# Performance work log

Measured on AMD Instinct MI355X. Metric: run time of the kernel, lower is better.

The kernel has to match this reference:

```python
import jax, jax.numpy as jnp
import numpy as np

# Static sizes (match input_specs / init_kwargs)
N = 10000       # nodes
E = 160000      # edges
L = 2           # num_layers
S = 256         # scalar_dim (hidden_dim)
V = 32          # vec_dim (1o and 1e channel count)
L2 = 16         # 2e channel count
NRBF = 16
TDIM = 128
ESD = NRBF + 16 + 20 + 8 + S + S + TDIM   # 700 edge-scalar dim
WOUT = S + 4 * V + L2                     # 400 per-edge TP path weights
ADA = 2 * S + 2 * V + L2                  # 592 AdaLN modulation dim
FEAT = S + 3 * V + 3 * V + 5 * L2         # 528 flattened irreps width
DEG_INV = 1.0 / np.sqrt(E / N)            # 1/sqrt(avg degree) message normalizer


def setup_inputs() -> dict:
    key = jax.random.key(0)
    ks = jax.random.split(key, 30)
    f32 = jnp.float32

    def nrm(k, shape, scale=1.0):
        return jax.random.normal(k, shape, dtype=f32) * scale

    inp = {
        "h": nrm(ks[0], (N, FEAT)),
        "coords": nrm(ks[1], (N, 3), 3.0),
        "edge_ref_dist": jax.random.uniform(ks[2], (E,), dtype=f32) * 4.0,
        "t_emb": nrm(ks[3], (N, TDIM)),
        # per-layer learned params, stacked on leading L axis
        "etype_emb": nrm(ks[4], (L, 9, 16), 0.5),
        "btype_emb": nrm(ks[5], (L, 6, 8), 0.5),
        "bconj_emb": nrm(ks[6], (L, 3, 4), 0.5),
        "bring_emb": nrm(ks[7], (L, 3, 4), 0.5),
        "bstereo_emb": nrm(ks[8], (L, 5, 4), 0.5),
        "ref_W": nrm(ks[9], (L, 3, 8), 1.0 / np.sqrt(3)),
        "ref_b": jnp.zeros((L, 8), f32),
        "edge_W": nrm(ks[10], (L, ESD, WOUT), 1.0 / np.sqrt(ESD)),
        "edge_b": jnp.zeros((L, WOUT), f32),
        "sv_W": nrm(ks[11], (L, S, V), 1.0 / np.sqrt(S)),
        "proj_s": nrm(ks[12], (L, S, S), 1.0 / np.sqrt(S)),
        "proj_v1": nrm(ks[13], (L, V, V), 1.0 / np.sqrt(V)),
        "proj_v2": nrm(ks[14], (L, V, V), 1.0 / np.sqrt(V)),
        "proj_l2": nrm(ks[15], (L, L2, L2), 1.0 / np.sqrt(L2)),
        "ada_W": nrm(ks[16], (L, TDIM, ADA), 1.0 / np.sqrt(TDIM)),
        "ada_b": jnp.zeros((L, ADA), f32),
        # int graph structure
        "edge_index": jax.random.randint(ks[17], (2, E), 0, N),
        "edge_type": jax.random.randint(ks[18], (E,), 0, 9),
        "edge_bond_type": jax.random.randint(ks[19], (E,), 0, 6),
        "edge_bond_conjugated": jax.random.randint(ks[20], (E,), 0, 3),
        "edge_bond_in_ring": jax.random.randint(ks[21], (E,), 0, 3),
        "edge_bond_stereo": jax.random.randint(ks[22], (E,), 0, 5),
    }
    return inp


def _forward(h, coords, edge_ref_dist, t_emb,
             etype_emb, btype_emb, bconj_emb, bring_emb, bstereo_emb,
             ref_W, ref_b, edge_W, edge_b, sv_W,
             proj_s, proj_v1, proj_v2, proj_l2, ada_W, ada_b,
             edge_index, edge_type, edge_bond_type,
             edge_bond_conjugated, edge_bond_in_ring, edge_bond_stereo):
    src, dst = edge_index[0], edge_index[1]
    # geometry (shared across layers)
    diff = coords[dst] - coords[src]                    # [E,3]
    dist = jnp.linalg.norm(diff, axis=-1)               # [E]
    centers = jnp.linspace(0.0, 10.0, NRBF)
    width = 10.0 / NRBF
    rbf = jnp.exp(-(((dist[:, None] - centers) / width) ** 2))   # [E,NRBF]
    Y1 = diff / (dist[:, None] + 1e-8)                  # unit direction, l=1 SH
    has_ref = (edge_ref_dist > 0).astype(jnp.float32)
    delta = dist - edge_ref_dist
    ref_feat = jnp.stack([jnp.abs(delta), delta, has_ref], axis=-1)  # [E,3]

    for l in range(L):
        # split irreps blocks
        s = h[:, :S]
        v1o = h[:, S:S + 3 * V].reshape(N, V, 3)
        v1e = h[:, S + 3 * V:S + 6 * V].reshape(N, V, 3)
        q2e = h[:, S + 6 * V:].reshape(N, L2, 5)

        # edge scalar features (embeddings + RBF + node scalars + time)
        e_type = etype_emb[l][edge_type]
        e_bond = jnp.concatenate([
            btype_emb[l][edge_bond_type], bconj_emb[l][edge_bond_conjugated],
            bring_emb[l][edge_bond_in_ring], bstereo_emb[l][edge_bond_stereo]], axis=-1)
        e_ref = ref_feat @ ref_W[l] + ref_b[l]
        edge_scalars = jnp.concatenate(
            [rbf, e_type, e_bond, e_ref, s[src], s[dst], t_emb[dst]], axis=-1)  # [E,700]

        # per-edge tensor-product path weights
        w = edge_scalars @ edge_W[l] + edge_b[l]          # [E,400]
        w_s, w_v1, w_sv, w_v2, w_cx, w_l2 = jnp.split(
            w, [S, S + V, S + 2 * V, S + 3 * V, S + 4 * V], axis=-1)

        sv = s @ sv_W[l]                                  # [N,V] scalar->vec gate channels
        # equivariant messages
        m_s = w_s * s[src]                                                   # 0e x 0e -> 0e
        m_v1o = w_v1[:, :, None] * v1o[src] \
              + (w_sv * sv[src])[:, :, None] * Y1[:, None, :]                # 0e x 1o -> 1o
        m_v1e = w_v2[:, :, None] * v1e[src] \
              + w_cx[:, :, None] * jnp.cross(v1o[src], Y1[:, None, :])       # 1o x 1o -> 1e
        m_l2 = w_l2[:, :, None] * q2e[src]                                   # 0e x 2e -> 2e

        # scatter-sum to destination nodes
        agg_s = jax.ops.segment_sum(m_s, dst, num_segments=N) * DEG_INV
        agg_v1o = jax.ops.segment_sum(m_v1o, dst, num_segments=N) * DEG_INV
        agg_v1e = jax.ops.segment_sum(m_v1e, dst, num_segments=N) * DEG_INV
        agg_l2 = jax.ops.segment_sum(m_l2, dst, num_segments=N) * DEG_INV

        # per-irrep channel-mixing projection, scalar activation
        u_s = jax.nn.silu(agg_s @ proj_s[l])
        u_v1o = jnp.einsum('nci,cd->ndi', agg_v1o, proj_v1[l])
        u_v1e = jnp.einsum('nci,cd->ndi', agg_v1e, proj_v2[l])
        u_l2 = jnp.einsum('nci,cd->ndi', agg_l2, proj_l2[l])

        # residual
        s = s + u_s
        v1o = v1o + u_v1o
        v1e = v1e + u_v1e
        q2e = q2e + u_l2

        # equivariant AdaLN conditioned on t_emb
        ada = t_emb @ ada_W[l] + ada_b[l]
        sc, sh_, g1, g2, gl = jnp.split(ada, [S, 2 * S, 2 * S + V, 2 * S + 2 * V], axis=-1)
        mu = s.mean(axis=-1, keepdims=True)
        var = s.var(axis=-1, keepdims=True)
        s = (s - mu) / jnp.sqrt(var + 1e-5) * (1.0 + sc) + sh_

        def vnorm(v, g):
            rms = jnp.sqrt(jnp.mean(jnp.sum(v * v, axis=-1), axis=-1, keepdims=True) + 1e-5)
            return v / rms[:, :, None] * (1.0 + g)[:, :, None]

        v1o = vnorm(v1o, g1)
        v1e = vnorm(v1e, g2)
        q2e = vnorm(q2e, gl)

        h = jnp.concatenate(
            [s, v1o.reshape(N, 3 * V), v1e.reshape(N, 3 * V), q2e.reshape(N, 5 * L2)], axis=-1)
    return h


def reference(h, coords, edge_ref_dist, t_emb,
              etype_emb, btype_emb, bconj_emb, bring_emb, bstereo_emb,
              ref_W, ref_b, edge_W, edge_b, sv_W,
              proj_s, proj_v1, proj_v2, proj_l2, ada_W, ada_b,
              edge_index, edge_type, edge_bond_type,
              edge_bond_conjugated, edge_bond_in_ring, edge_bond_stereo):
    return _forward(h, coords, edge_ref_dist, t_emb,
                    etype_emb, btype_emb, bconj_emb, bring_emb, bstereo_emb,
                    ref_W, ref_b, edge_W, edge_b, sv_W,
                    proj_s, proj_v1, proj_v2, proj_l2, ada_W, ada_b,
                    edge_index, edge_type, edge_bond_type,
                    edge_bond_conjugated, edge_bond_in_ring, edge_bond_stereo)
```

## Files before the change

### kernel.cpp

```cpp
#include <hip/hip_runtime.h>
#include <math.h>

#define NN 10000
#define NE 160000
#define SDIM 256
#define VDIM 32
#define L2DIM 16
#define TDIM 128
#define FEAT 528
#define WOUT 400
#define ADA 592
#define DEG_INV 0.25f

#define ETM 16
#define WLP 404
#define AP1 72
#define AP2 392
#define AP3 264
#define HSP 536

typedef short bf16x8 __attribute__((ext_vector_type(8)));
typedef float f32x4 __attribute__((ext_vector_type(4)));

__device__ __forceinline__ unsigned short f2bf(float f) {
    unsigned int u = __float_as_uint(f);
    u += 0x7fffu + ((u >> 16) & 1u);
    return (unsigned short)(u >> 16);
}
__device__ __forceinline__ float bf2f(unsigned short b) {
    return __uint_as_float(((unsigned int)b) << 16);
}

__global__ __launch_bounds__(256) void hist_kernel(const int* __restrict__ eidx,
                                                   int* __restrict__ cnt) {
    int e = blockIdx.x * 256 + threadIdx.x;
    if (e < NE) atomicAdd(&cnt[eidx[NE + e]], 1);
}

__global__ __launch_bounds__(1024) void scan_kernel(const int* __restrict__ cnt,
                                                    int* __restrict__ cursor) {
    __shared__ int sc[1024];
    int tid = threadIdx.x;
    int base = tid * 10;
    int loc[10];
    int s = 0;
    if (base < NN) {
        #pragma unroll
        for (int j = 0; j < 10; ++j) { loc[j] = cnt[base + j]; s += loc[j]; }
    }
    sc[tid] = s;
    __syncthreads();
    for (int off = 1; off < 1024; off <<= 1) {
        int v = sc[tid];
        int add = (tid >= off) ? sc[tid - off] : 0;
        __syncthreads();
        sc[tid] = v + add;
        __syncthreads();
    }
    int run = sc[tid] - s;
    if (base < NN) {
        #pragma unroll
        for (int j = 0; j < 10; ++j) { cursor[base + j] = run; run += loc[j]; }
    }
}

__global__ __launch_bounds__(256) void scatter_kernel(const int* __restrict__ eidx,
                                                      int* __restrict__ cursor,
                                                      int* __restrict__ perm) {
    int e = blockIdx.x * 256 + threadIdx.x;
    if (e < NE) {
        int d = eidx[NE + e];
        int p = atomicAdd(&cursor[d], 1);
        perm[p] = e;
    }
}

#define O1 25600
#define O2 332800
#define O3 408576
#define O4 416768
#define O5 482304
__global__ __launch_bounds__(256) void prep_kernel(
    const float* __restrict__ W, const float* __restrict__ adaW,
    const float* __restrict__ svW, const float* __restrict__ projs,
    unsigned short* __restrict__ Wt1, unsigned short* __restrict__ Bn,
    unsigned short* __restrict__ Ba, unsigned short* __restrict__ Bsv,
    unsigned short* __restrict__ Ps)
{
    int idx = blockIdx.x * 256 + threadIdx.x;
    if (idx < O1) {
        int c = idx >> 6, k = idx & 63;
        float v = (k < 60) ? W[(size_t)k * WOUT + c] : 0.f;
        Wt1[idx] = f2bf(v);
    } else if (idx < O2) {
        int i = idx - O1;
        int c = i / 384, k = i - c * 384;
        float v;
        if (c < WOUT) v = (k < 256) ? W[(size_t)(60 + k) * WOUT + c] : 0.f;
        else {
            int c2 = c - WOUT;
            v = (k < 256) ? W[(size_t)(316 + k) * WOUT + c2]
                          : W[(size_t)(572 + (k - 256)) * WOUT + c2];
        }
        Bn[i] = f2bf(v);
    } else if (idx < O3) {
        int i = idx - O2;
        int c = i >> 7, k = i & 127;
        Ba[i] = f2bf(adaW[(size_t)k * ADA + c]);
    } else if (idx < O4) {
        int i = idx - O3;
        int c = i >> 8, k = i & 255;
        Bsv[i] = f2bf(svW[(size_t)k * VDIM + c]);
    } else if (idx < O5) {
        int i = idx - O4;
        int c = i >> 8, k = i & 255;
        Ps[i] = f2bf(projs[(size_t)k * SDIM + c]);
    }
}

struct us4 { unsigned short x, y, z, w; };
__global__ __launch_bounds__(256) void hb_kernel(const float* __restrict__ h,
                                                 unsigned short* __restrict__ hb) {
    int i = blockIdx.x * 256 + threadIdx.x;
    if (i >= NN * FEAT / 4) return;
    float4 v = ((const float4*)h)[i];
    us4 o;
    o.x = f2bf(v.x); o.y = f2bf(v.y); o.z = f2bf(v.z); o.w = f2bf(v.w);
    ((us4*)hb)[i] = o;
}

__global__ __launch_bounds__(256) void nodeproj_kernel(
    const unsigned short* __restrict__ hb, const float* __restrict__ t_emb,
    const unsigned short* __restrict__ Bn, const unsigned short* __restrict__ Ba,
    const unsigned short* __restrict__ Bsv,
    const float* __restrict__ edge_b, const float* __restrict__ adab,
    unsigned short* __restrict__ srcdst, float* __restrict__ ada_out,
    float* __restrict__ sv)
{
    __shared__ unsigned short As2[32 * AP2];
    const int tid = threadIdx.x;
    const int n0 = blockIdx.x * 32;

    for (int e = 0; e < 32; ++e) {
        int n = n0 + e;
        As2[e * AP2 + tid] = (n < NN) ? hb[(size_t)n * FEAT + tid] : 0;
        if (tid < 128) {
            float v1 = (n < NN) ? t_emb[(size_t)n * TDIM + tid] : 0.f;
            As2[e * AP2 + 256 + tid] = f2bf(v1);
        }
    }
    __syncthreads();

    const int wid = tid >> 6, lane = tid & 63;
    const int lr = lane & 15, lkb = (lane >> 4) << 3;
    const int rbase = (lane >> 4) << 2;

    {
        const int nt0 = wid * 13;
        f32x4 acc[2][13];
        #pragma unroll
        for (int m = 0; m < 2; ++m)
            #pragma unroll
            for (int t = 0; t < 13; ++t) acc[m][t] = (f32x4){0.f, 0.f, 0.f, 0.f};

        for (int ks = 0; ks < 12; ++ks) {
            int kb = ks * 32 + lkb;
            bf16x8 a0 = *(const bf16x8*)&As2[lr * AP2 + kb];
            bf16x8 a1 = *(const bf16x8*)&As2[(16 + lr) * AP2 + kb];
            #pragma unroll
            for (int t = 0; t < 13; ++t) {
                int tile = nt0 + t;
                if (tile < 50) {
                    bf16x8 b = *(const bf16x8*)&Bn[(size_t)(tile * 16 + lr) * 384 + kb];
                    acc[0][t] = __builtin_amdgcn_mfma_f32_16x16x32_bf16(a0, b, acc[0][t], 0, 0, 0);
                    acc[1][t] = __builtin_amdgcn_mfma_f32_16x16x32_bf16(a1, b, acc[1][t], 0, 0, 0);
                }
            }
        }
        #pragma unroll
        for (int t = 0; t < 13; ++t) {
            int tile = nt0 + t;
            if (tile < 50) {
                int col = tile * 16 + lr;
                float badd = (col >= WOUT) ? edge_b[col - WOUT] : 0.f;
                #pragma unroll
                for (int m = 0; m < 2; ++m) {
                    #pragma unroll
                    for (int r = 0; r < 4; ++r) {
                        int n = n0 + m * 16 + rbase + r;
                        if (n < NN) srcdst[(size_t)n * 800 + col] = f2bf(acc[m][t][r] + badd);
                    }
                }
            }
        }
    }

    {
        const int nt0a = wid * 9;
        f32x4 acc2[2][10];
        #pragma unroll
        for (int m = 0; m < 2; ++m)
            #pragma unroll
            for (int t = 0; t < 10; ++t) acc2[m][t] = (f32x4){0.f, 0.f, 0.f, 0.f};

        for (int ks = 0; ks < 4; ++ks) {
            int kin = ks * 32 + lkb;
            bf16x8 a0 = *(const bf16x8*)&As2[lr * AP2 + 256 + kin];
            bf16x8 a1 = *(const bf16x8*)&As2[(16 + lr) * AP2 + 256 + kin];
            #pragma unroll
            for (int t = 0; t < 10; ++t) {
                int tile = nt0a + t;
                if (tile < 37) {
                    bf16x8 b = *(const bf16x8*)&Ba[(size_t)(tile * 16 + lr) * 128 + kin];
                    acc2[0][t] = __builtin_amdgcn_mfma_f32_16x16x32_bf16(a0, b, acc2[0][t], 0, 0, 0);
                    acc2[1][t] = __builtin_amdgcn_mfma_f32_16x16x32_bf16(a1, b, acc2[1][t], 0, 0, 0);
                }
            }
        }
        #pragma unroll
        for (int t = 0; t < 10; ++t) {
            int tile = nt0a + t;
            if (tile < 37) {
                int col = tile * 16 + lr;
                float badd = adab[col];
                #pragma unroll
                for (int m = 0; m < 2; ++m) {
                    #pragma unroll
                    for (int r = 0; r < 4; ++r) {
                        int n = n0 + m * 16 + rbase + r;
                        if (n < NN) ada_out[(size_t)n * ADA + col] = acc2[m][t][r] + badd;
                    }
                }
            }
        }
    }

    if (wid < 2) {
        f32x4 accs[2];
        accs[0] = (f32x4){0.f, 0.f, 0.f, 0.f};
        accs[1] = (f32x4){0.f, 0.f, 0.f, 0.f};
        for (int ks = 0; ks < 8; ++ks) {
            int kb = ks * 32 + lkb;
            bf16x8 a0 = *(const bf16x8*)&As2[lr * AP2 + kb];
            bf16x8 a1 = *(const bf16x8*)&As2[(16 + lr) * AP2 + kb];
            bf16x8 b = *(const bf16x8*)&Bsv[(size_t)(wid * 16 + lr) * 256 + kb];
            accs[0] = __builtin_amdgcn_mfma_f32_16x16x32_bf16(a0, b, accs[0], 0, 0, 0);
            accs[1] = __builtin_amdgcn_mfma_f32_16x16x32_bf16(a1, b, accs[1], 0, 0, 0);
        }
        int col = wid * 16 + lr;
        #pragma unroll
        for (int m = 0; m < 2; ++m) {
            #pragma unroll
            for (int r = 0; r < 4; ++r) {
                int n = n0 + m * 16 + rbase + r;
                if (n < NN) sv[(size_t)n * VDIM + col] = accs[m][r];
            }
        }
    }
}

__global__ __launch_bounds__(256) void edge_kernel(
    const unsigned short* __restrict__ hb, const float* __restrict__ coords,
    const float* __restrict__ erd, const float* __restrict__ sv,
    const unsigned short* __restrict__ Wt1, const unsigned short* __restrict__ srcdst,
    const int* __restrict__ perm, const int* __restrict__ eidx,
    const int* __restrict__ etype, const int* __restrict__ ebt,
    const int* __restrict__ ebc, const int* __restrict__ ebr,
    const int* __restrict__ ebs,
    const float* __restrict__ etype_emb, const float* __restrict__ btype_emb,
    const float* __restrict__ bconj_emb, const float* __restrict__ bring_emb,
    const float* __restrict__ bstereo_emb,
    const float* __restrict__ refW, const float* __restrict__ refb,
    float* __restrict__ agg)
{
    __shared__ unsigned short wl[ETM * WLP];
    __shared__ unsigned short hsl[ETM * HSP];
    __shared__ float svl[ETM * VDIM];
    __shared__ unsigned short As[ETM * AP1];
    __shared__ int srcl[ETM], dstl[ETM];
    __shared__ int itype[ETM], ibt[ETM], ibc[ETM], ibr[ETM], ibs[ETM];
    __shared__ float distl[ETM], erdl[ETM], y1l[ETM][3];

    const int tid = threadIdx.x;
    const int e0 = blockIdx.x * ETM;

    if (tid < ETM) {
        int ge = perm[e0 + tid];
        int s = eidx[ge], d = eidx[NE + ge];
        srcl[tid] = s; dstl[tid] = d;
        itype[tid] = etype[ge]; ibt[tid] = ebt[ge]; ibc[tid] = ebc[ge];
        ibr[tid] = ebr[ge]; ibs[tid] = ebs[ge];
        float dx = coords[d*3+0] - coords[s*3+0];
        float dy = coords[d*3+1] - coords[s*3+1];
        float dz = coords[d*3+2] - coords[s*3+2];
        float dist = sqrtf(dx*dx + dy*dy + dz*dz);
        distl[tid] = dist;
        float inv = 1.f / (dist + 1e-8f);
        y1l[tid][0] = dx * inv; y1l[tid][1] = dy * inv; y1l[tid][2] = dz * inv;
        erdl[tid] = erd[ge];
    }
    __syncthreads();

    {
        for (int i = tid; i < ETM * 66; i += 256) {
            int e = i / 66, j = i - e * 66;
            bf16x8 v = *(const bf16x8*)&hb[(size_t)srcl[e] * FEAT + j * 8];
            *(bf16x8*)&hsl[e * HSP + j * 8] = v;
        }
        for (int i = tid; i < ETM * VDIM; i += 256) {
            int e = i >> 5, c = i & 31;
            svl[i] = sv[(size_t)srcl[e] * VDIM + c];
        }
    }

    {
        const int k = tid & 63;
        const int ebase = tid >> 6;
        #pragma unroll
        for (int it = 0; it < 4; ++it) {
            int e = it * 4 + ebase;
            float de = distl[e];
            float v;
            if (k >= 60) v = 0.f;
            else if (k < 16) { float x = (de - (float)k * (10.f/15.f)) * 1.6f; v = expf(-x*x); }
            else if (k < 32) v = etype_emb[itype[e]*16 + (k-16)];
            else if (k < 40) v = btype_emb[ibt[e]*8 + (k-32)];
            else if (k < 44) v = bconj_emb[ibc[e]*4 + (k-40)];
            else if (k < 48) v = bring_emb[ibr[e]*4 + (k-44)];
            else if (k < 52) v = bstereo_emb[ibs[e]*4 + (k-48)];
            else {
                int j = k - 52;
                float dd = de - erdl[e];
                float hr = erdl[e] > 0.f ? 1.f : 0.f;
                v = fabsf(dd)*refW[j] + dd*refW[8+j] + hr*refW[16+j] + refb[j];
            }
            As[e * AP1 + k] = f2bf(v);
        }
    }
    __syncthreads();

    const int wid = tid >> 6, lane = tid & 63;
    const int lr = lane & 15, lkb = (lane >> 4) << 3;
    const int nt0 = wid * 6;
    {
        f32x4 acc[7];
        #pragma unroll
        for (int t = 0; t < 7; ++t) acc[t] = (f32x4){0.f, 0.f, 0.f, 0.f};

        #pragma unroll
        for (int ks = 0; ks < 2; ++ks) {
            int kb = ks * 32 + lkb;
            bf16x8 a0 = *(const bf16x8*)&As[lr * AP1 + kb];
            #pragma unroll
            for (int t = 0; t < 7; ++t) {
                bf16x8 b = *(const bf16x8*)&Wt1[(size_t)((nt0 + t) * 16 + lr) * 64 + kb];
                acc[t] = __builtin_amdgcn_mfma_f32_16x16x32_bf16(a0, b, acc[t], 0, 0, 0);
            }
        }
        const int rbase = (lane >> 4) << 2;
        int se[4];
        #pragma unroll
        for (int r = 0; r < 4; ++r) se[r] = srcl[rbase + r];
        #pragma unroll
        for (int t = 0; t < 7; ++t) {
            const int col = (nt0 + t) * 16 + lr;
            #pragma unroll
            for (int r = 0; r < 4; ++r) {
                float add = bf2f(srcdst[(size_t)se[r] * 800 + col]);
                wl[(rbase + r) * WLP + col] = f2bf(acc[t][r] + add);
            }
        }
    }
    __syncthreads();

    {
        int cls = 0, cc = 0, ii = 0, ia = 0, ib = 0, hoff = 0, wB1 = 0, wB2 = 0;
        if (tid < 96)       { cls = 0; cc = tid / 3;        ii = tid % 3;        hoff = 256 + tid; wB1 = 256 + cc; wB2 = 288 + cc; }
        else if (tid < 192) { int j = tid - 96; cls = 1; cc = j / 3; ii = j % 3; hoff = 352 + j;   wB1 = 320 + cc; wB2 = 352 + cc; }
        else                { int j = tid - 192; cls = 2; cc = j / 5;            hoff = 448 + j;   wB1 = 384 + cc; }
        ia = (ii + 1) % 3; ib = (ii + 2) % 3;

        const bool hasC = tid < 16;
        const int jC = 64 + tid;
        const int hoffC = 448 + jC;
        const int wC = 384 + jC / 5;

        float accA = 0.f, accAs = 0.f;
        float accB = 0.f, accB1 = 0.f, accB2 = 0.f;
        float accC = 0.f, accC1 = 0.f;
        for (int e = 0; e < ETM; ++e) {
            const unsigned short* hs = &hsl[e * HSP];
            float sA = bf2f(hs[tid]);
            accA = fmaf(bf2f(wl[e * WLP + tid]), sA, accA);
            accAs += sA;
            float m;
            if (cls == 0) {
                float wv1 = bf2f(wl[e * WLP + wB1]), wsv = bf2f(wl[e * WLP + wB2]);
                float a = bf2f(hs[hoff]);
                float svy = svl[e * VDIM + cc] * y1l[e][ii];
                m = wv1 * a + wsv * svy;
                accB1 += a; accB2 += svy;
            } else if (cls == 1) {
                float wv2 = bf2f(wl[e * WLP + wB1]), wcx = bf2f(wl[e * WLP + wB2]);
                float a = bf2f(hs[hoff]);
                float va = bf2f(hs[256 + cc * 3 + ia]), vb = bf2f(hs[256 + cc * 3 + ib]);
                float cr = va * y1l[e][ib] - vb * y1l[e][ia];
                m = wv2 * a + wcx * cr;
                accB1 += a; accB2 += cr;
            } else {
                float a = bf2f(hs[hoff]);
                m = bf2f(wl[e * WLP + wB1]) * a;
                accB1 += a;
            }
            accB += m;
            if (hasC) {
                float aC = bf2f(hs[hoffC]);
                accC = fmaf(bf2f(wl[e * WLP + wC]), aC, accC);
                accC1 += aC;
            }

            bool fl = (e == ETM - 1) || (dstl[e + 1] != dstl[e]);
            if (fl) {
                int d = dstl[e];
                const unsigned short* wd = &srcdst[(size_t)d * 800 + 400];
                atomicAdd(&agg[(size_t)d * FEAT + tid], accA + bf2f(wd[tid]) * accAs);
                float bout;
                if (cls == 2) bout = accB + bf2f(wd[wB1]) * accB1;
                else          bout = accB + bf2f(wd[wB1]) * accB1 + bf2f(wd[wB2]) * accB2;
                atomicAdd(&agg[(size_t)d * FEAT + 256 + tid], bout);
                if (hasC) atomicAdd(&agg[(size_t)d * FEAT + hoffC], accC + bf2f(wd[wC]) * accC1);
                accA = 0.f; accAs = 0.f; accB = 0.f; accB1 = 0.f; accB2 = 0.f;
                accC = 0.f; accC1 = 0.f;
            }
        }
    }
}

__global__ __launch_bounds__(256) void proj_kernel(
    const float* __restrict__ agg, const unsigned short* __restrict__ Ps,
    unsigned short* __restrict__ us_buf)
{
    __shared__ unsigned short As3[32 * AP3];
    const int tid = threadIdx.x;
    const int n0 = blockIdx.x * 32;

    for (int e = 0; e < 32; ++e) {
        int n = n0 + e;
        float v = (n < NN) ? agg[(size_t)n * FEAT + tid] * DEG_INV : 0.f;
        As3[e * AP3 + tid] = f2bf(v);
    }
    __syncthreads();

    const int wid = tid >> 6, lane = tid & 63;
    const int lr = lane & 15, lkb = (lane >> 4) << 3;
    const int rbase = (lane >> 4) << 2;
    const int nt0 = wid * 4;

    f32x4 acc[2][4];
    #pragma unroll
    for (int m = 0; m < 2; ++m)
        #pragma unroll
        for (int t = 0; t < 4; ++t) acc[m][t] = (f32x4){0.f, 0.f, 0.f, 0.f};

    for (int ks = 0; ks < 8; ++ks) {
        int kb = ks * 32 + lkb;
        bf16x8 a0 = *(const bf16x8*)&As3[lr * AP3 + kb];
        bf16x8 a1 = *(const bf16x8*)&As3[(16 + lr) * AP3 + kb];
        #pragma unroll
        for (int t = 0; t < 4; ++t) {
            bf16x8 b = *(const bf16x8*)&Ps[(size_t)((nt0 + t) * 16 + lr) * 256 + kb];
            acc[0][t] = __builtin_amdgcn_mfma_f32_16x16x32_bf16(a0, b, acc[0][t], 0, 0, 0);
            acc[1][t] = __builtin_amdgcn_mfma_f32_16x16x32_bf16(a1, b, acc[1][t], 0, 0, 0);
        }
    }
    #pragma unroll
    for (int t = 0; t < 4; ++t) {
        int col = (nt0 + t) * 16 + lr;
        #pragma unroll
        for (int m = 0; m < 2; ++m) {
            #pragma unroll
            for (int r = 0; r < 4; ++r) {
                int n = n0 + m * 16 + rbase + r;
                if (n < NN) {
                    float x = acc[m][t][r];
                    us_buf[(size_t)n * SDIM + col] = f2bf(x / (1.f + expf(-x)));
                }
            }
        }
    }
}

__global__ __launch_bounds__(256) void node_kernel(
    const float* __restrict__ hcur, const float* __restrict__ ada_buf,
    const float* __restrict__ agg, const unsigned short* __restrict__ us_buf,
    const float* __restrict__ pv1, const float* __restrict__ pv2,
    const float* __restrict__ pl2,
    float* __restrict__ hnext, unsigned short* __restrict__ hbnext)
{
    __shared__ float plv1[VDIM * VDIM];
    __shared__ float plv2[VDIM * VDIM];
    __shared__ float pll2[L2DIM * L2DIM];
    __shared__ float avl[4][272];

    const int tid = threadIdx.x;
    for (int i = tid; i < VDIM * VDIM; i += 256) { plv1[i] = pv1[i]; plv2[i] = pv2[i]; }
    if (tid < L2DIM * L2DIM) pll2[tid] = pl2[tid];

    const int w = tid >> 6, lane = tid & 63;
    const int n = blockIdx.x * 4 + w;
    const size_t nb = (size_t)n * FEAT;
    const size_t na = (size_t)n * ADA;

    for (int i = lane; i < 272; i += 64) avl[w][i] = agg[nb + 256 + i] * DEG_INV;
    __syncthreads();

    float snv[4];
    float ssum = 0.f, ssq = 0.f;
    #pragma unroll
    for (int j = 0; j < 4; ++j) {
        int c = lane + 64 * j;
        float v = hcur[nb + c] + bf2f(us_buf[(size_t)n * SDIM + c]);
        snv[j] = v; ssum += v; ssq += v * v;
    }
    #pragma unroll
    for (int off = 32; off > 0; off >>= 1) {
        ssum += __shfl_xor(ssum, off, 64);
        ssq  += __shfl_xor(ssq, off, 64);
    }
    float mu = ssum * (1.f / SDIM);
    float var = ssq * (1.f / SDIM) - mu * mu;
    float rstd = rsqrtf(var + 1e-5f);
    #pragma unroll
    for (int j = 0; j < 4; ++j) {
        int c = lane + 64 * j;
        float o = (snv[j] - mu) * rstd * (1.f + ada_buf[na + c]) + ada_buf[na + SDIM + c];
        hnext[nb + c] = o;
        if (hbnext) hbnext[nb + c] = f2bf(o);
    }

    float vb[5];
    float S1 = 0.f, S2 = 0.f, S3 = 0.f;
    #pragma unroll
    for (int j = 0; j < 5; ++j) {
        int c = (j < 4) ? (lane + 64 * j) : (256 + lane);
        bool ok = (j < 4) || (lane < 16);
        float val = 0.f;
        if (ok) {
            if (c < 96) {
                int d = c / 3, i = c - 3 * d;
                float a = 0.f;
                #pragma unroll
                for (int k = 0; k < VDIM; ++k) a = fmaf(avl[w][k*3 + i], plv1[k * VDIM + d], a);
                val = hcur[nb + SDIM + c] + a;
                S1 += val * val;
            } else if (c < 192) {
                int c2 = c - 96;
                int d = c2 / 3, i = c2 - 3 * d;
                float a = 0.f;
                #pragma unroll
                for (int k = 0; k < VDIM; ++k) a = fmaf(avl[w][96 + k*3 + i], plv2[k * VDIM + d], a);
                val = hcur[nb + SDIM + c] + a;
                S2 += val * val;
            } else {
                int c2 = c - 192;
                int d = c2 / 5, i = c2 - 5 * d;
                float a = 0.f;
                #pragma unroll
                for (int k = 0; k < L2DIM; ++k) a = fmaf(avl[w][192 + k*5 + i], pll2[k * L2DIM + d], a);
                val = hcur[nb + SDIM + c] + a;
                S3 += val * val;
            }
        }
        vb[j] = val;
    }
    #pragma unroll
    for (int off = 32; off > 0; off >>= 1) {
        S1 += __shfl_xor(S1, off, 64);
        S2 += __shfl_xor(S2, off, 64);
        S3 += __shfl_xor(S3, off, 64);
    }
    float r1 = rsqrtf(S1 * (1.f / VDIM) + 1e-5f);
    float r2 = rsqrtf(S2 * (1.f / VDIM) + 1e-5f);
    float r3 = rsqrtf(S3 * (1.f / L2DIM) + 1e-5f);

    #pragma unroll
    for (int j = 0; j < 5; ++j) {
        int c = (j < 4) ? (lane + 64 * j) : (256 + lane);
        bool ok = (j < 4) || (lane < 16);
        if (ok) {
            float o;
            if (c < 96) {
                int d = c / 3;
                o = vb[j] * r1 * (1.f + ada_buf[na + 2*SDIM + d]);
            } else if (c < 192) {
                int d = (c - 96) / 3;
                o = vb[j] * r2 * (1.f + ada_buf[na + 2*SDIM + VDIM + d]);
            } else {
                int d = (c - 192) / 5;
                o = vb[j] * r3 * (1.f + ada_buf[na + 2*SDIM + 2*VDIM + d]);
            }
            hnext[nb + SDIM + c] = o;
            if (hbnext) hbnext[nb + SDIM + c] = f2bf(o);
        }
    }
}

extern "C" void kernel_launch(void* const* d_in, const int* in_sizes, int n_in,
                              void* d_out, int out_size, void* d_ws, size_t ws_size,
                              hipStream_t stream) {
    const float* h_in   = (const float*)d_in[0];
    const float* coords = (const float*)d_in[1];
    const float* erd    = (const float*)d_in[2];
    const float* t_emb  = (const float*)d_in[3];
    const float* etype_emb   = (const float*)d_in[4];
    const float* btype_emb   = (const float*)d_in[5];
    const float* bconj_emb   = (const float*)d_in[6];
    const float* bring_emb   = (const float*)d_in[7];
    const float* bstereo_emb = (const float*)d_in[8];
    const float* refW   = (const float*)d_in[9];
    const float* refb   = (const float*)d_in[10];
    const float* edgeW  = (const float*)d_in[11];
    const float* edgeb  = (const float*)d_in[12];
    const float* svW    = (const float*)d_in[13];
    const float* proj_s = (const float*)d_in[14];
    const float* proj_v1= (const float*)d_in[15];
    const float* proj_v2= (const float*)d_in[16];
    const float* proj_l2= (const float*)d_in[17];
    const float* adaW   = (const float*)d_in[18];
    const float* adab   = (const float*)d_in[19];
    const int* eidx     = (const int*)d_in[20];
    const int* etype    = (const int*)d_in[21];
    const int* ebt      = (const int*)d_in[22];
    const int* ebc      = (const int*)d_in[23];
    const int* ebr      = (const int*)d_in[24];
    const int* ebs      = (const int*)d_in[25];

    float* ws_f     = (float*)d_ws;
    float* sv       = ws_f;
    float* agg      = sv + (size_t)NN * VDIM;
    float* h1       = agg + (size_t)NN * FEAT;
    float* ada_buf  = h1 + (size_t)NN * FEAT;
    float* us_f     = ada_buf + (size_t)NN * ADA;
    unsigned short* us_buf = (unsigned short*)us_f;
    unsigned short* srcdst = (unsigned short*)(us_f + (size_t)NN * SDIM);
    unsigned short* hb     = srcdst + (size_t)NN * 800;
    unsigned short* Wt1    = hb + (size_t)NN * FEAT;
    unsigned short* Bn     = Wt1 + (size_t)WOUT * 64;
    unsigned short* Ba     = Bn + (size_t)800 * 384;
    unsigned short* Bsv    = Ba + (size_t)ADA * 128;
    unsigned short* Ps     = Bsv + (size_t)VDIM * 256;
    int* cnt    = (int*)(Ps + (size_t)SDIM * 256);
    int* cursor = cnt + NN;
    int* perm   = cursor + NN;

    hipMemsetAsync(cnt, 0, NN * sizeof(int), stream);
    hist_kernel<<<(NE + 255) / 256, 256, 0, stream>>>(eidx, cnt);
    scan_kernel<<<1, 1024, 0, stream>>>(cnt, cursor);
    scatter_kernel<<<(NE + 255) / 256, 256, 0, stream>>>(eidx, cursor, perm);
    hb_kernel<<<(NN * FEAT / 4 + 255) / 256, 256, 0, stream>>>(h_in, hb);

    for (int l = 0; l < 2; ++l) {
        const float* hcur = (l == 0) ? h_in : h1;
        float* hnext      = (l == 0) ? h1 : (float*)d_out;
        const float* W    = edgeW + (size_t)l * 700 * WOUT;

        hipMemsetAsync(agg, 0, (size_t)NN * FEAT * sizeof(float), stream);
        prep_kernel<<<(O5 + 255) / 256, 256, 0, stream>>>(
            W, adaW + (size_t)l * TDIM * ADA, svW + (size_t)l * SDIM * VDIM,
            proj_s + (size_t)l * SDIM * SDIM, Wt1, Bn, Ba, Bsv, Ps);
        nodeproj_kernel<<<(NN + 31) / 32, 256, 0, stream>>>(
            hb, t_emb, Bn, Ba, Bsv, edgeb + l * WOUT, adab + l * ADA,
            srcdst, ada_buf, sv);
        edge_kernel<<<NE / ETM, 256, 0, stream>>>(
            hb, coords, erd, sv, Wt1, srcdst, perm,
            eidx, etype, ebt, ebc, ebr, ebs,
            etype_emb + l * 144, btype_emb + l * 48, bconj_emb + l * 12,
            bring_emb + l * 12, bstereo_emb + l * 20,
            refW + l * 24, refb + l * 8,
            agg);
        proj_kernel<<<(NN + 31) / 32, 256, 0, stream>>>(agg, Ps, us_buf);
        node_kernel<<<NN / 4, 256, 0, stream>>>(
            hcur, ada_buf, agg, us_buf,
            proj_v1 + l * VDIM * VDIM, proj_v2 + l * VDIM * VDIM,
            proj_l2 + l * L2DIM * L2DIM,
            hnext, (l == 0) ? hb : (unsigned short*)nullptr);
    }
}
```

Measured before the change: 774.6 us.

## Assign one block per destination node and drop atomic aggregation

The edge kernel now launches one block per destination node and loops over that node's incoming edges in chunks of 16, using the CSR row offsets saved by the scan. The destination part of the edge weights is added per edge before the tensor-product step, and each node's result is written directly instead of accumulated with atomics. This removes the memset of the aggregation buffer and the atomic traffic. In exchange, nodes with few incoming edges leave chunks partly idle, and load balance follows the degree distribution.

```diff
diff --git a/kernel.cpp b/kernel.cpp
--- a/kernel.cpp
+++ b/kernel.cpp
@@ -38,7 +38,8 @@
 }
 
 __global__ __launch_bounds__(1024) void scan_kernel(const int* __restrict__ cnt,
-                                                    int* __restrict__ cursor) {
+                                                    int* __restrict__ cursor,
+                                                    int* __restrict__ rowstart) {
     __shared__ int sc[1024];
     int tid = threadIdx.x;
     int base = tid * 10;
@@ -60,7 +61,11 @@
     int run = sc[tid] - s;
     if (base < NN) {
         #pragma unroll
-        for (int j = 0; j < 10; ++j) { cursor[base + j] = run; run += loc[j]; }
+        for (int j = 0; j < 10; ++j) {
+            cursor[base + j] = run;
+            rowstart[base + j] = run;
+            run += loc[j];
+        }
     }
 }
 
@@ -263,7 +268,8 @@
     const unsigned short* __restrict__ hb, const float* __restrict__ coords,
     const float* __restrict__ erd, const float* __restrict__ sv,
     const unsigned short* __restrict__ Wt1, const unsigned short* __restrict__ srcdst,
-    const int* __restrict__ perm, const int* __restrict__ eidx,
+    const int* __restrict__ perm, const int* __restrict__ rowstart,
+    const int* __restrict__ cntv, const int* __restrict__ eidx,
     const int* __restrict__ etype, const int* __restrict__ ebt,
     const int* __restrict__ ebc, const int* __restrict__ ebr,
     const int* __restrict__ ebs,
@@ -277,163 +283,161 @@
     __shared__ unsigned short hsl[ETM * HSP];
     __shared__ float svl[ETM * VDIM];
     __shared__ unsigned short As[ETM * AP1];
-    __shared__ int srcl[ETM], dstl[ETM];
+    __shared__ float wdl[WOUT];
+    __shared__ int srcl[ETM];
     __shared__ int itype[ETM], ibt[ETM], ibc[ETM], ibr[ETM], ibs[ETM];
     __shared__ float distl[ETM], erdl[ETM], y1l[ETM][3];
 
     const int tid = threadIdx.x;
-    const int e0 = blockIdx.x * ETM;
-
-    if (tid < ETM) {
-        int ge = perm[e0 + tid];
-        int s = eidx[ge], d = eidx[NE + ge];
-        srcl[tid] = s; dstl[tid] = d;
-        itype[tid] = etype[ge]; ibt[tid] = ebt[ge]; ibc[tid] = ebc[ge];
-        ibr[tid] = ebr[ge]; ibs[tid] = ebs[ge];
-        float dx = coords[d*3+0] - coords[s*3+0];
-        float dy = coords[d*3+1] - coords[s*3+1];
-        float dz = coords[d*3+2] - coords[s*3+2];
-        float dist = sqrtf(dx*dx + dy*dy + dz*dz);
-        distl[tid] = dist;
-        float inv = 1.f / (dist + 1e-8f);
-        y1l[tid][0] = dx * inv; y1l[tid][1] = dy * inv; y1l[tid][2] = dz * inv;
-        erdl[tid] = erd[ge];
-    }
-    __syncthreads();
+    const int d = blockIdx.x;
+    const int ebeg = rowstart[d];
+    const int ecnt = cntv[d];
 
     {
-        for (int i = tid; i < ETM * 66; i += 256) {
+        const unsigned short* wd = &srcdst[(size_t)d * 800 + 400];
+        if (tid < 200) {
+            wdl[tid] = bf2f(wd[tid]);
+            wdl[200 + tid] = bf2f(wd[200 + tid]);
+        }
+    }
+    float cdx = coords[d * 3 + 0], cdy = coords[d * 3 + 1], cdz = coords[d * 3 + 2];
+
+    int cls = 0, cc = 0, ii = 0, ia = 0, ib = 0, hoff = 0, wB1 = 0, wB2 = 0;
+    if (tid < 96)       { cls = 0; cc = tid / 3;        ii = tid % 3;        hoff = 256 + tid; wB1 = 256 + cc; wB2 = 288 + cc; }
+    else if (tid < 192) { int j = tid - 96; cls = 1; cc = j / 3; ii = j % 3; hoff = 352 + j;   wB1 = 320 + cc; wB2 = 352 + cc; }
+    else                { int j = tid - 192; cls = 2; cc = j / 5;            hoff = 448 + j;   wB1 = 384 + cc; }
+    ia = (ii + 1) % 3; ib = (ii + 2) % 3;
+    const bool hasC = tid < 16;
+    const int jC = 64 + tid;
+    const int hoffC = 448 + jC;
+    const int wC = 384 + jC / 5;
+
+    const int wid = tid >> 6, lane = tid & 63;
+    const int lr = lane & 15, lkb = (lane >> 4) << 3;
+    const int nt0 = wid * 6;
+    const int rbase = (lane >> 4) << 2;
+
+    float accA = 0.f, accB = 0.f, accC = 0.f;
+
+    const int nch = (ecnt + ETM - 1) / ETM;
+    for (int ch = 0; ch < nch; ++ch) {
+        const int ec = min(ETM, ecnt - ch * ETM);
+        __syncthreads();
+
+        if (tid < ETM) {
+            if (tid < ec) {
+                int ge = perm[ebeg + ch * ETM + tid];
+                int s = eidx[ge];
+                srcl[tid] = s;
+                itype[tid] = etype[ge]; ibt[tid] = ebt[ge]; ibc[tid] = ebc[ge];
+                ibr[tid] = ebr[ge]; ibs[tid] = ebs[ge];
+                float dx = cdx - coords[s*3+0];
+                float dy = cdy - coords[s*3+1];
+                float dz = cdz - coords[s*3+2];
+                float dist = sqrtf(dx*dx + dy*dy + dz*dz);
+                distl[tid] = dist;
+                float inv = 1.f / (dist + 1e-8f);
+                y1l[tid][0] = dx * inv; y1l[tid][1] = dy * inv; y1l[tid][2] = dz * inv;
+                erdl[tid] = erd[ge];
+            } else {
+                srcl[tid] = 0;
+            }
+        }
+        __syncthreads();
+
+        for (int i = tid; i < ec * 66; i += 256) {
             int e = i / 66, j = i - e * 66;
             bf16x8 v = *(const bf16x8*)&hb[(size_t)srcl[e] * FEAT + j * 8];
             *(bf16x8*)&hsl[e * HSP + j * 8] = v;
         }
-        for (int i = tid; i < ETM * VDIM; i += 256) {
+        for (int i = tid; i < ec * VDIM; i += 256) {
             int e = i >> 5, c = i & 31;
             svl[i] = sv[(size_t)srcl[e] * VDIM + c];
         }
-    }
-
-    {
-        const int k = tid & 63;
-        const int ebase = tid >> 6;
-        #pragma unroll
-        for (int it = 0; it < 4; ++it) {
-            int e = it * 4 + ebase;
-            float de = distl[e];
-            float v;
-            if (k >= 60) v = 0.f;
-            else if (k < 16) { float x = (de - (float)k * (10.f/15.f)) * 1.6f; v = expf(-x*x); }
-            else if (k < 32) v = etype_emb[itype[e]*16 + (k-16)];
-            else if (k < 40) v = btype_emb[ibt[e]*8 + (k-32)];
-            else if (k < 44) v = bconj_emb[ibc[e]*4 + (k-40)];
-            else if (k < 48) v = bring_emb[ibr[e]*4 + (k-44)];
-            else if (k < 52) v = bstereo_emb[ibs[e]*4 + (k-48)];
-            else {
-                int j = k - 52;
-                float dd = de - erdl[e];
-                float hr = erdl[e] > 0.f ? 1.f : 0.f;
-                v = fabsf(dd)*refW[j] + dd*refW[8+j] + hr*refW[16+j] + refb[j];
-            }
-            As[e * AP1 + k] = f2bf(v);
-        }
-    }
-    __syncthreads();
-
-    const int wid = tid >> 6, lane = tid & 63;
-    const int lr = lane & 15, lkb = (lane >> 4) << 3;
-    const int nt0 = wid * 6;
-    {
-        f32x4 acc[7];
-        #pragma unroll
-        for (int t = 0; t < 7; ++t) acc[t] = (f32x4){0.f, 0.f, 0.f, 0.f};
-
-        #pragma unroll
-        for (int ks = 0; ks < 2; ++ks) {
-            int kb = ks * 32 + lkb;
-            bf16x8 a0 = *(const bf16x8*)&As[lr * AP1 + kb];
+
+        {
+            const int k = tid & 63;
+            const int ebase = tid >> 6;
+            #pragma unroll
+            for (int it = 0; it < 4; ++it) {
+                int e = it * 4 + ebase;
+                if (e < ec) {
+                    float de = distl[e];
+                    float v;
+                    if (k >= 60) v = 0.f;
+                    else if (k < 16) { float x = (de - (float)k * (10.f/15.f)) * 1.6f; v = expf(-x*x); }
+                    else if (k < 32) v = etype_emb[itype[e]*16 + (k-16)];
+                    else if (k < 40) v = btype_emb[ibt[e]*8 + (k-32)];
+                    else if (k < 44) v = bconj_emb[ibc[e]*4 + (k-40)];
+                    else if (k < 48) v = bring_emb[ibr[e]*4 + (k-44)];
+                    else if (k < 52) v = bstereo_emb[ibs[e]*4 + (k-48)];
+                    else {
+                        int j = k - 52;
+                        float dd = de - erdl[e];
+                        float hr = erdl[e] > 0.f ? 1.f : 0.f;
+                        v = fabsf(dd)*refW[j] + dd*refW[8+j] + hr*refW[16+j] + refb[j];
+                    }
+                    As[e * AP1 + k] = f2bf(v);
+                } else {
+                    As[e * AP1 + k] = 0;
+                }
+            }
+        }
+        __syncthreads();
+
+        {
+            f32x4 acc[7];
+            #pragma unroll
+            for (int t = 0; t < 7; ++t) acc[t] = (f32x4){0.f, 0.f, 0.f, 0.f};
+
+            #pragma unroll
+            for (int ks = 0; ks < 2; ++ks) {
+                int kb = ks * 32 + lkb;
+                bf16x8 a0 = *(const bf16x8*)&As[lr * AP1 + kb];
+                #pragma unroll
+                for (int t = 0; t < 7; ++t) {
+                    bf16x8 b = *(const bf16x8*)&Wt1[(size_t)((nt0 + t) * 16 + lr) * 64 + kb];
+                    acc[t] = __builtin_amdgcn_mfma_f32_16x16x32_bf16(a0, b, acc[t], 0, 0, 0);
+                }
+            }
+            int se[4];
+            #pragma unroll
+            for (int r = 0; r < 4; ++r) se[r] = srcl[rbase + r];
             #pragma unroll
             for (int t = 0; t < 7; ++t) {
-                bf16x8 b = *(const bf16x8*)&Wt1[(size_t)((nt0 + t) * 16 + lr) * 64 + kb];
-                acc[t] = __builtin_amdgcn_mfma_f32_16x16x32_bf16(a0, b, acc[t], 0, 0, 0);
-            }
-        }
-        const int rbase = (lane >> 4) << 2;
-        int se[4];
-        #pragma unroll
-        for (int r = 0; r < 4; ++r) se[r] = srcl[rbase + r];
-        #pragma unroll
-        for (int t = 0; t < 7; ++t) {
-            const int col = (nt0 + t) * 16 + lr;
-            #pragma unroll
-            for (int r = 0; r < 4; ++r) {
-                float add = bf2f(srcdst[(size_t)se[r] * 800 + col]);
-                wl[(rbase + r) * WLP + col] = f2bf(acc[t][r] + add);
-            }
-        }
-    }
-    __syncthreads();
-
-    {
-        int cls = 0, cc = 0, ii = 0, ia = 0, ib = 0, hoff = 0, wB1 = 0, wB2 = 0;
-        if (tid < 96)       { cls = 0; cc = tid / 3;        ii = tid % 3;        hoff = 256 + tid; wB1 = 256 + cc; wB2 = 288 + cc; }
-        else if (tid < 192) { int j = tid - 96; cls = 1; cc = j / 3; ii = j % 3; hoff = 352 + j;   wB1 = 320 + cc; wB2 = 352 + cc; }
-        else                { int j = tid - 192; cls = 2; cc = j / 5;            hoff = 448 + j;   wB1 = 384 + cc; }
-        ia = (ii + 1) % 3; ib = (ii + 2) % 3;
-
-        const bool hasC = tid < 16;
-        const int jC = 64 + tid;
-        const int hoffC = 448 + jC;
-        const int wC = 384 + jC / 5;
-
-        float accA = 0.f, accAs = 0.f;
-        float accB = 0.f, accB1 = 0.f, accB2 = 0.f;
-        float accC = 0.f, accC1 = 0.f;
-        for (int e = 0; e < ETM; ++e) {
+                const int col = (nt0 + t) * 16 + lr;
+                const float wdv = wdl[col];
+                #pragma unroll
+                for (int r = 0; r < 4; ++r) {
+                    float add = bf2f(srcdst[(size_t)se[r] * 800 + col]) + wdv;
+                    wl[(rbase + r) * WLP + col] = f2bf(acc[t][r] + add);
+                }
+            }
+        }
+        __syncthreads();
+
+        for (int e = 0; e < ec; ++e) {
             const unsigned short* hs = &hsl[e * HSP];
-            float sA = bf2f(hs[tid]);
-            accA = fmaf(bf2f(wl[e * WLP + tid]), sA, accA);
-            accAs += sA;
+            accA = fmaf(bf2f(wl[e * WLP + tid]), bf2f(hs[tid]), accA);
             float m;
             if (cls == 0) {
                 float wv1 = bf2f(wl[e * WLP + wB1]), wsv = bf2f(wl[e * WLP + wB2]);
-                float a = bf2f(hs[hoff]);
-                float svy = svl[e * VDIM + cc] * y1l[e][ii];
-                m = wv1 * a + wsv * svy;
-                accB1 += a; accB2 += svy;
+                m = wv1 * bf2f(hs[hoff]) + wsv * svl[e * VDIM + cc] * y1l[e][ii];
             } else if (cls == 1) {
                 float wv2 = bf2f(wl[e * WLP + wB1]), wcx = bf2f(wl[e * WLP + wB2]);
-                float a = bf2f(hs[hoff]);
                 float va = bf2f(hs[256 + cc * 3 + ia]), vb = bf2f(hs[256 + cc * 3 + ib]);
-                float cr = va * y1l[e][ib] - vb * y1l[e][ia];
-                m = wv2 * a + wcx * cr;
-                accB1 += a; accB2 += cr;
+                m = wv2 * bf2f(hs[hoff]) + wcx * (va * y1l[e][ib] - vb * y1l[e][ia]);
             } else {
-                float a = bf2f(hs[hoff]);
-                m = bf2f(wl[e * WLP + wB1]) * a;
-                accB1 += a;
+                m = bf2f(wl[e * WLP + wB1]) * bf2f(hs[hoff]);
             }
             accB += m;
-            if (hasC) {
-                float aC = bf2f(hs[hoffC]);
-                accC = fmaf(bf2f(wl[e * WLP + wC]), aC, accC);
-                accC1 += aC;
-            }
-
-            bool fl = (e == ETM - 1) || (dstl[e + 1] != dstl[e]);
-            if (fl) {
-                int d = dstl[e];
-                const unsigned short* wd = &srcdst[(size_t)d * 800 + 400];
-                atomicAdd(&agg[(size_t)d * FEAT + tid], accA + bf2f(wd[tid]) * accAs);
-                float bout;
-                if (cls == 2) bout = accB + bf2f(wd[wB1]) * accB1;
-                else          bout = accB + bf2f(wd[wB1]) * accB1 + bf2f(wd[wB2]) * accB2;
-                atomicAdd(&agg[(size_t)d * FEAT + 256 + tid], bout);
-                if (hasC) atomicAdd(&agg[(size_t)d * FEAT + hoffC], accC + bf2f(wd[wC]) * accC1);
-                accA = 0.f; accAs = 0.f; accB = 0.f; accB1 = 0.f; accB2 = 0.f;
-                accC = 0.f; accC1 = 0.f;
-            }
-        }
-    }
+            if (hasC) accC = fmaf(bf2f(wl[e * WLP + wC]), bf2f(hs[hoffC]), accC);
+        }
+    }
+
+    agg[(size_t)d * FEAT + tid] = accA;
+    agg[(size_t)d * FEAT + hoff] = accB;
+    if (hasC) agg[(size_t)d * FEAT + hoffC] = accC;
 }
 
 __global__ __launch_bounds__(256) void proj_kernel(
@@ -649,13 +653,14 @@
     unsigned short* Ba     = Bn + (size_t)800 * 384;
     unsigned short* Bsv    = Ba + (size_t)ADA * 128;
     unsigned short* Ps     = Bsv + (size_t)VDIM * 256;
-    int* cnt    = (int*)(Ps + (size_t)SDIM * 256);
-    int* cursor = cnt + NN;
-    int* perm   = cursor + NN;
+    int* cnt      = (int*)(Ps + (size_t)SDIM * 256);
+    int* cursor   = cnt + NN;
+    int* rowstart = cursor + NN;
+    int* perm     = rowstart + NN;
 
     hipMemsetAsync(cnt, 0, NN * sizeof(int), stream);
     hist_kernel<<<(NE + 255) / 256, 256, 0, stream>>>(eidx, cnt);
-    scan_kernel<<<1, 1024, 0, stream>>>(cnt, cursor);
+    scan_kernel<<<1, 1024, 0, stream>>>(cnt, cursor, rowstart);
     scatter_kernel<<<(NE + 255) / 256, 256, 0, stream>>>(eidx, cursor, perm);
     hb_kernel<<<(NN * FEAT / 4 + 255) / 256, 256, 0, stream>>>(h_in, hb);
 
@@ -664,15 +669,14 @@
         float* hnext      = (l == 0) ? h1 : (float*)d_out;
         const float* W    = edgeW + (size_t)l * 700 * WOUT;
 
-        hipMemsetAsync(agg, 0, (size_t)NN * FEAT * sizeof(float), stream);
         prep_kernel<<<(O5 + 255) / 256, 256, 0, stream>>>(
             W, adaW + (size_t)l * TDIM * ADA, svW + (size_t)l * SDIM * VDIM,
             proj_s + (size_t)l * SDIM * SDIM, Wt1, Bn, Ba, Bsv, Ps);
         nodeproj_kernel<<<(NN + 31) / 32, 256, 0, stream>>>(
             hb, t_emb, Bn, Ba, Bsv, edgeb + l * WOUT, adab + l * ADA,
             srcdst, ada_buf, sv);
-        edge_kernel<<<NE / ETM, 256, 0, stream>>>(
-            hb, coords, erd, sv, Wt1, srcdst, perm,
+        edge_kernel<<<NN, 256, 0, stream>>>(
+            hb, coords, erd, sv, Wt1, srcdst, perm, rowstart, cnt,
             eidx, etype, ebt, ebc, ebr, ebs,
             etype_emb + l * 144, btype_emb + l * 48, bconj_emb + l * 12,
             bring_emb + l * 12, bstereo_emb + l * 20,
```

Result: slower. 1.051 ms (+35.7%).

## Fold destination weight term into edge weights and swizzle block order

Applied to the files above, without the earlier changes.

The per-destination part of the edge weights is now added directly to each edge's weight row in the GEMM epilogue. Previously it was applied at flush time through separate sums of the inputs, which needed extra accumulators and reads of the destination row. This removes several accumulators and flush-time reads, at the cost of one more gather per weight element. The block index is also remapped so that consecutive hardware blocks are spread across eight strided chunks of edges, likely to spread work or atomics across XCDs/caches.

```diff
diff --git a/kernel.cpp b/kernel.cpp
--- a/kernel.cpp
+++ b/kernel.cpp
@@ -282,7 +282,8 @@
     __shared__ float distl[ETM], erdl[ETM], y1l[ETM][3];
 
     const int tid = threadIdx.x;
-    const int e0 = blockIdx.x * ETM;
+    const int bid = (blockIdx.x & 7) * 1250 + (blockIdx.x >> 3);
+    const int e0 = bid * ETM;
 
     if (tid < ETM) {
         int ge = perm[e0 + tid];
@@ -358,15 +359,16 @@
             }
         }
         const int rbase = (lane >> 4) << 2;
-        int se[4];
-        #pragma unroll
-        for (int r = 0; r < 4; ++r) se[r] = srcl[rbase + r];
+        int se[4], de_[4];
+        #pragma unroll
+        for (int r = 0; r < 4; ++r) { se[r] = srcl[rbase + r]; de_[r] = dstl[rbase + r]; }
         #pragma unroll
         for (int t = 0; t < 7; ++t) {
             const int col = (nt0 + t) * 16 + lr;
             #pragma unroll
             for (int r = 0; r < 4; ++r) {
-                float add = bf2f(srcdst[(size_t)se[r] * 800 + col]);
+                float add = bf2f(srcdst[(size_t)se[r] * 800 + col])
+                          + bf2f(srcdst[(size_t)de_[r] * 800 + 400 + col]);
                 wl[(rbase + r) * WLP + col] = f2bf(acc[t][r] + add);
             }
         }
@@ -385,52 +387,31 @@
         const int hoffC = 448 + jC;
         const int wC = 384 + jC / 5;
 
-        float accA = 0.f, accAs = 0.f;
-        float accB = 0.f, accB1 = 0.f, accB2 = 0.f;
-        float accC = 0.f, accC1 = 0.f;
+        float accA = 0.f, accB = 0.f, accC = 0.f;
         for (int e = 0; e < ETM; ++e) {
             const unsigned short* hs = &hsl[e * HSP];
-            float sA = bf2f(hs[tid]);
-            accA = fmaf(bf2f(wl[e * WLP + tid]), sA, accA);
-            accAs += sA;
+            accA = fmaf(bf2f(wl[e * WLP + tid]), bf2f(hs[tid]), accA);
             float m;
             if (cls == 0) {
                 float wv1 = bf2f(wl[e * WLP + wB1]), wsv = bf2f(wl[e * WLP + wB2]);
-                float a = bf2f(hs[hoff]);
-                float svy = svl[e * VDIM + cc] * y1l[e][ii];
-                m = wv1 * a + wsv * svy;
-                accB1 += a; accB2 += svy;
+                m = wv1 * bf2f(hs[hoff]) + wsv * svl[e * VDIM + cc] * y1l[e][ii];
             } else if (cls == 1) {
                 float wv2 = bf2f(wl[e * WLP + wB1]), wcx = bf2f(wl[e * WLP + wB2]);
-                float a = bf2f(hs[hoff]);
                 float va = bf2f(hs[256 + cc * 3 + ia]), vb = bf2f(hs[256 + cc * 3 + ib]);
-                float cr = va * y1l[e][ib] - vb * y1l[e][ia];
-                m = wv2 * a + wcx * cr;
-                accB1 += a; accB2 += cr;
+                m = wv2 * bf2f(hs[hoff]) + wcx * (va * y1l[e][ib] - vb * y1l[e][ia]);
             } else {
-                float a = bf2f(hs[hoff]);
-                m = bf2f(wl[e * WLP + wB1]) * a;
-                accB1 += a;
+                m = bf2f(wl[e * WLP + wB1]) * bf2f(hs[hoff]);
             }
             accB += m;
-            if (hasC) {
-                float aC = bf2f(hs[hoffC]);
-                accC = fmaf(bf2f(wl[e * WLP + wC]), aC, accC);
-                accC1 += aC;
-            }
+            if (hasC) accC = fmaf(bf2f(wl[e * WLP + wC]), bf2f(hs[hoffC]), accC);
 
             bool fl = (e == ETM - 1) || (dstl[e + 1] != dstl[e]);
             if (fl) {
                 int d = dstl[e];
-                const unsigned short* wd = &srcdst[(size_t)d * 800 + 400];
-                atomicAdd(&agg[(size_t)d * FEAT + tid], accA + bf2f(wd[tid]) * accAs);
-                float bout;
-                if (cls == 2) bout = accB + bf2f(wd[wB1]) * accB1;
-                else          bout = accB + bf2f(wd[wB1]) * accB1 + bf2f(wd[wB2]) * accB2;
-                atomicAdd(&agg[(size_t)d * FEAT + 256 + tid], bout);
-                if (hasC) atomicAdd(&agg[(size_t)d * FEAT + hoffC], accC + bf2f(wd[wC]) * accC1);
-                accA = 0.f; accAs = 0.f; accB = 0.f; accB1 = 0.f; accB2 = 0.f;
-                accC = 0.f; accC1 = 0.f;
+                atomicAdd(&agg[(size_t)d * FEAT + tid], accA);
+                atomicAdd(&agg[(size_t)d * FEAT + 256 + tid], accB);
+                if (hasC) atomicAdd(&agg[(size_t)d * FEAT + hoffC], accC);
+                accA = 0.f; accB = 0.f; accC = 0.f;
             }
         }
     }
```

After: 748.9 us. 3.3% less time.
